# Kernel optimization log

Hardware: AMD Instinct MI355X
Metric: run time of the kernel (lower is better)

## Reference

```python
import jax, jax.numpy as jnp
import numpy as np

B, S, NX = 2, 2048, 1024
N_STATE, N_HEAD = 1024, 16
HEAD_DIM = N_STATE // N_HEAD


def setup_inputs() -> dict:
    key = jax.random.key(0)
    k1, k2, k3 = jax.random.split(key, 3)
    x = jax.random.normal(k1, (B, S, NX), dtype=jnp.float32)
    w_c = jax.random.normal(k2, (NX, 3 * N_STATE), dtype=jnp.float32) * 0.02
    b_c = jnp.zeros((3 * N_STATE,), dtype=jnp.float32)
    w_p = jax.random.normal(k3, (NX, N_STATE), dtype=jnp.float32) * 0.02
    b_p = jnp.zeros((N_STATE,), dtype=jnp.float32)
    return {"x": x, "w_c": w_c, "b_c": b_c, "w_p": w_p, "b_p": b_p}


def reference(x, w_c, b_c, w_p, b_p):
    # c_attn: 1x1 conv == dense over last dim -> [B, S, 3*n_state]
    c = jnp.einsum('bsn,nf->bsf', x, w_c) + b_c
    q, k, v = jnp.split(c, 3, axis=2)

    def split_heads(t):  # [B,S,n_state] -> [B,H,S,D]
        return t.reshape(B, S, N_HEAD, HEAD_DIM).transpose(0, 2, 1, 3)

    q = split_heads(q)
    k = split_heads(k)  # we contract over D directly instead of transposing to [B,H,D,S]
    v = split_heads(v)

    # scores [B,H,S,S], scaled by rsqrt(head_dim) (scale=True)
    w = jnp.einsum('bhqd,bhkd->bhqk', q, k) * jax.lax.rsqrt(jnp.float32(HEAD_DIM))
    # band mask exactly as in source: w*b + -1e9*(1-b)
    band = jnp.tril(jnp.ones((S, S), dtype=jnp.float32))[None, None]
    w = w * band + (-1e9) * (1.0 - band)
    w = jax.nn.softmax(w, axis=-1)
    a = jnp.einsum('bhqk,bhkd->bhqd', w, v)

    # merge heads -> [B,S,n_state]
    a = a.transpose(0, 2, 1, 3).reshape(B, S, N_STATE)
    # c_proj
    out = jnp.einsum('bsn,nf->bsf', a, w_p) + b_p
    return out
```

## Files before the change

kernel.cpp:

```cpp
#include <hip/hip_runtime.h>
#include <math.h>

#define BATCH 2
#define SEQ 2048
#define NX 1024
#define NSTATE 1024
#define NHEAD 16
#define HDIM 64
#define QKV_LD (3*NSTATE)

typedef __attribute__((ext_vector_type(4))) float f32x4;
typedef __attribute__((ext_vector_type(8))) short bf16x8;

__device__ __forceinline__ unsigned short f2bf(float x) {
    unsigned int u = __float_as_uint(x);
    u = (u + 0x7FFFu + ((u >> 16) & 1u)) >> 16;
    return (unsigned short)u;
}

__device__ __forceinline__ unsigned int cvtpk_bf16(float a, float b) {
    unsigned int r;
    asm("v_cvt_pk_bf16_f32 %0, %1, %2" : "=v"(r) : "v"(a), "v"(b));
    return r;
}

#define GLL(src, dst) __builtin_amdgcn_global_load_lds( \
    (const __attribute__((address_space(1))) void*)(src), \
    (__attribute__((address_space(3))) void*)(dst), 16, 0, 0)

__global__ __launch_bounds__(256) void prep_kernel(
    const float* __restrict__ x, const float* __restrict__ w_c,
    const float* __restrict__ w_p,
    unsigned short* __restrict__ xbf, unsigned short* __restrict__ wcT,
    unsigned short* __restrict__ wpT)
{
    const int bx = blockIdx.x;
    const int t = threadIdx.x;
    if (bx < 4096) {
        int i = bx * 256 + t;
        float4 v = ((const float4*)x)[i];
        ushort4 o;
        o.x = f2bf(v.x); o.y = f2bf(v.y); o.z = f2bf(v.z); o.w = f2bf(v.w);
        ((ushort4*)xbf)[i] = o;
        return;
    }
    __shared__ float tile[64][65];
    const float* in;
    unsigned short* out;
    int R, C, c0, r0;
    if (bx < 4096 + 768) {
        int idx = bx - 4096;
        in = w_c; out = wcT; R = NX; C = 3 * NSTATE;
        c0 = (idx % 48) * 64; r0 = (idx / 48) * 64;
    } else {
        int idx = bx - 4864;
        in = w_p; out = wpT; R = NX; C = NSTATE;
        c0 = (idx % 16) * 64; r0 = (idx / 16) * 64;
    }
    const int cc = t & 63;
    const int rb = t >> 6;
    #pragma unroll
    for (int i = 0; i < 16; i++) {
        int rr = rb + i * 4;
        tile[rr][cc] = in[(size_t)(r0 + rr) * C + c0 + cc];
    }
    __syncthreads();
    #pragma unroll
    for (int i = 0; i < 16; i++) {
        int rr = rb + i * 4;
        out[(size_t)(c0 + rr) * R + r0 + cc] = f2bf(tile[cc][rr]);
    }
}

__global__ __launch_bounds__(256) void vtrans_kernel(
    const unsigned short* __restrict__ qkv, unsigned short* __restrict__ vt)
{
    __shared__ unsigned short t[64][72];
    const int s0 = blockIdx.x * 64;
    const int bh = blockIdx.y;
    const int b = bh >> 4, h = bh & 15;
    const int r = threadIdx.x >> 2;
    const int cg = (threadIdx.x & 3) * 16;
    const unsigned short* src = qkv + (size_t)(b * SEQ + s0 + r) * QKV_LD
                                + 2 * NSTATE + h * HDIM + cg;
    *(bf16x8*)&t[r][cg]     = *(const bf16x8*)src;
    *(bf16x8*)&t[r][cg + 8] = *(const bf16x8*)(src + 8);
    __syncthreads();
    unsigned short tmp[16];
    #pragma unroll
    for (int i = 0; i < 16; i++) tmp[i] = t[cg + i][r];
    unsigned short* dst = vt + (size_t)(bh * 64 + r) * SEQ + s0 + cg;
    *(bf16x8*)dst       = ((const bf16x8*)tmp)[0];
    *(bf16x8*)(dst + 8) = ((const bf16x8*)tmp)[1];
}

template<bool BF16_OUT>
__global__ __launch_bounds__(256) void gemm_bf16(
    const unsigned short* __restrict__ A,
    const unsigned short* __restrict__ BT,
    const float* __restrict__ bias,
    void* __restrict__ Cv, int M, int N, int K)
{
    __shared__ unsigned short Als[128 * 32];
    __shared__ unsigned short Bls[128 * 32];
    const int tid = threadIdx.x;
    const int wave = tid >> 6, lane = tid & 63;
    const int bm = blockIdx.x * 128, bn = blockIdx.y * 128;
    const int wr = (wave >> 1) * 64, wc = (wave & 1) * 64;

    f32x4 acc[4][4];
    #pragma unroll
    for (int m = 0; m < 4; m++)
        #pragma unroll
        for (int n = 0; n < 4; n++)
            acc[m][n] = (f32x4){0.f, 0.f, 0.f, 0.f};

    const int arow = tid >> 2;
    const int ac8 = (tid & 3) * 8;
    char* alds0 = (char*)Als + wave * 1024;
    char* blds0 = (char*)Bls + wave * 1024;
    const int fr = lane & 15, kq = (lane >> 4) * 8;

    for (int k0 = 0; k0 < K; k0 += 32) {
        const unsigned short* ga0 = A  + (size_t)(bm + arow) * K + k0 + ac8;
        const unsigned short* gb0 = BT + (size_t)(bn + arow) * K + k0 + ac8;
        GLL(ga0, alds0);
        GLL(ga0 + (size_t)64 * K, alds0 + 4096);
        GLL(gb0, blds0);
        GLL(gb0 + (size_t)64 * K, blds0 + 4096);
        __syncthreads();

        bf16x8 af[4], bfr[4];
        #pragma unroll
        for (int m = 0; m < 4; m++)
            af[m] = *(const bf16x8*)&Als[(wr + m * 16 + fr) * 32 + kq];
        #pragma unroll
        for (int n = 0; n < 4; n++)
            bfr[n] = *(const bf16x8*)&Bls[(wc + n * 16 + fr) * 32 + kq];
        #pragma unroll
        for (int m = 0; m < 4; m++)
            #pragma unroll
            for (int n = 0; n < 4; n++)
                acc[m][n] = __builtin_amdgcn_mfma_f32_16x16x32_bf16(
                    af[m], bfr[n], acc[m][n], 0, 0, 0);
        __syncthreads();
    }

    const int cr = (lane >> 4) * 4;
    const int ccol = lane & 15;
    #pragma unroll
    for (int m = 0; m < 4; m++) {
        const int row = bm + wr + m * 16 + cr;
        #pragma unroll
        for (int n = 0; n < 4; n++) {
            const int col = bn + wc + n * 16 + ccol;
            const float bv = bias[col];
            #pragma unroll
            for (int j = 0; j < 4; j++) {
                float v = acc[m][n][j] + bv;
                if (BF16_OUT)
                    ((unsigned short*)Cv)[(size_t)(row + j) * N + col] = f2bf(v);
                else
                    ((float*)Cv)[(size_t)(row + j) * N + col] = v;
            }
        }
    }
}

__global__ __launch_bounds__(128) void attn_mfma(
    const unsigned short* __restrict__ qkv,
    const unsigned short* __restrict__ vt,
    unsigned short* __restrict__ a_out)
{
    const int cx = blockIdx.x;
    const int h = blockIdx.y, b = blockIdx.z;
    const int tid = threadIdx.x;
    const int w = tid >> 6, lane = tid & 63;
    const int c = lane & 15, hh = lane >> 4;

    __shared__ unsigned short Kls[2 * 64 * 64];
    __shared__ unsigned short Pls[2][16 * 64];

    const float Cc = 0.18033688f;

    const int rr = w * 8 + (lane >> 3);
    const int sc = ((lane & 7) * 16) ^ (((lane >> 3) & 7) << 4);

    const char* gkbase = (const char*)(qkv + (size_t)b * SEQ * QKV_LD + NSTATE + h * HDIM);
    const unsigned short* gv = vt + (size_t)(b * NHEAD + h) * HDIM * SEQ;

    #define STAGE(kt_, buf_) do { \
        const char* gk = gkbase + (size_t)(kt_) * 64 * 6144 + sc; \
        char* kd = (char*)Kls + (buf_) * 8192 + w * 1024; \
        GLL(gk + (size_t)(rr +  0) * 6144, kd); \
        GLL(gk + (size_t)(rr + 16) * 6144, kd + 2048); \
        GLL(gk + (size_t)(rr + 32) * 6144, kd + 4096); \
        GLL(gk + (size_t)(rr + 48) * 6144, kd + 6144); \
    } while (0)

    for (int phase = 0; phase < 2; phase++) {
        const int chunk = phase ? cx : (63 - cx);
        const int rowoff = (chunk & 1) * 32;
        const int qtile = chunk >> 1;

        const size_t qrow = (size_t)(b * SEQ + chunk * 32 + w * 16 + c);
        const unsigned short* qp = qkv + qrow * QKV_LD + h * HDIM;
        bf16x8 qf0 = *(const bf16x8*)(qp + hh * 8);
        bf16x8 qf1 = *(const bf16x8*)(qp + 32 + hh * 8);

        f32x4 acc_o[4];
        #pragma unroll
        for (int n = 0; n < 4; n++) acc_o[n] = (f32x4){0.f, 0.f, 0.f, 0.f};
        float m_run = -1e30f, l = 0.f;

        const int nkt = qtile + 1;
        STAGE(0, 0);
        __syncthreads();

        for (int kt = 0; kt < nkt; kt++) {
            const int cur = kt & 1;
            if (kt + 1 < nkt) STAGE(kt + 1, cur ^ 1);

            bf16x8 vf[4][2];
            #pragma unroll
            for (int n = 0; n < 4; n++)
                #pragma unroll
                for (int hf = 0; hf < 2; hf++)
                    vf[n][hf] = *(const bf16x8*)(gv + (size_t)(n * 16 + c) * SEQ
                                                 + kt * 64 + hf * 32 + hh * 8);

            const char* kb = (const char*)Kls + cur * 8192;

            f32x4 sacc[4];
            __builtin_amdgcn_s_setprio(1);
            #pragma unroll
            for (int m = 0; m < 4; m++) {
                const int row = m * 16 + c;
                const int sw = (row & 7) << 4;
                bf16x8 kf0 = *(const bf16x8*)(kb + row * 128 + ((hh * 16) ^ sw));
                bf16x8 kf1 = *(const bf16x8*)(kb + row * 128 + ((64 + hh * 16) ^ sw));
                f32x4 z = (f32x4){0.f, 0.f, 0.f, 0.f};
                z = __builtin_amdgcn_mfma_f32_16x16x32_bf16(kf0, qf0, z, 0, 0, 0);
                sacc[m] = __builtin_amdgcn_mfma_f32_16x16x32_bf16(kf1, qf1, z, 0, 0, 0);
            }
            __builtin_amdgcn_s_setprio(0);

            const bool diag = (kt == qtile);
            float s[16];
            #pragma unroll
            for (int m = 0; m < 4; m++)
                #pragma unroll
                for (int j = 0; j < 4; j++) {
                    float sv = sacc[m][j];
                    if (diag) {
                        int klocal = m * 16 + hh * 4 + j;
                        if (klocal > rowoff + w * 16 + c) sv = -1e30f;
                    }
                    s[m * 4 + j] = sv;
                }
            float x0 = fmaxf(s[0], s[1]),  x1 = fmaxf(s[2], s[3]);
            float x2 = fmaxf(s[4], s[5]),  x3 = fmaxf(s[6], s[7]);
            float x4 = fmaxf(s[8], s[9]),  x5 = fmaxf(s[10], s[11]);
            float x6 = fmaxf(s[12], s[13]), x7 = fmaxf(s[14], s[15]);
            float y0 = fmaxf(x0, x1), y1 = fmaxf(x2, x3);
            float y2 = fmaxf(x4, x5), y3 = fmaxf(x6, x7);
            float pmax = fmaxf(fmaxf(y0, y1), fmaxf(y2, y3));
            pmax = fmaxf(pmax, __shfl_xor(pmax, 16));
            pmax = fmaxf(pmax, __shfl_xor(pmax, 32));

            if (!__all(pmax <= m_run + 64.0f)) {
                const float mnew = fmaxf(m_run, pmax);
                const float alpha = exp2f((m_run - mnew) * Cc);
                m_run = mnew;
                l *= alpha;
                const float a0 = __shfl(alpha, hh * 4 + 0);
                const float a1 = __shfl(alpha, hh * 4 + 1);
                const float a2 = __shfl(alpha, hh * 4 + 2);
                const float a3 = __shfl(alpha, hh * 4 + 3);
                #pragma unroll
                for (int n = 0; n < 4; n++) {
                    acc_o[n][0] *= a0; acc_o[n][1] *= a1;
                    acc_o[n][2] *= a2; acc_o[n][3] *= a3;
                }
            }
            const float mc = m_run * Cc;
            float p[16];
            #pragma unroll
            for (int i = 0; i < 16; i++)
                p[i] = exp2f(fmaf(s[i], Cc, -mc));
            {
                float a0 = p[0] + p[1],  a1 = p[2] + p[3];
                float a2 = p[4] + p[5],  a3 = p[6] + p[7];
                float a4 = p[8] + p[9],  a5 = p[10] + p[11];
                float a6 = p[12] + p[13], a7 = p[14] + p[15];
                float b0 = a0 + a1, b1 = a2 + a3, b2 = a4 + a5, b3 = a6 + a7;
                l += (b0 + b1) + (b2 + b3);
            }

            {
                char* pb = (char*)&Pls[w][0] + c * 128;
                const int swp = (c & 7) << 4;
                #pragma unroll
                for (int m = 0; m < 4; m++) {
                    uint2 u;
                    u.x = cvtpk_bf16(p[m * 4 + 0], p[m * 4 + 1]);
                    u.y = cvtpk_bf16(p[m * 4 + 2], p[m * 4 + 3]);
                    *(uint2*)(pb + ((m * 32 + hh * 8) ^ swp)) = u;
                }
            }

            {
                const char* pb = (const char*)&Pls[w][0] + c * 128;
                const int swp = (c & 7) << 4;
                bf16x8 pf0 = *(const bf16x8*)(pb + ((hh * 16) ^ swp));
                bf16x8 pf1 = *(const bf16x8*)(pb + ((64 + hh * 16) ^ swp));
                __builtin_amdgcn_s_setprio(1);
                #pragma unroll
                for (int n = 0; n < 4; n++) {
                    acc_o[n] = __builtin_amdgcn_mfma_f32_16x16x32_bf16(pf0, vf[n][0], acc_o[n], 0, 0, 0);
                    acc_o[n] = __builtin_amdgcn_mfma_f32_16x16x32_bf16(pf1, vf[n][1], acc_o[n], 0, 0, 0);
                }
                __builtin_amdgcn_s_setprio(0);
            }
            __syncthreads();
        }

        l += __shfl_xor(l, 16);
        l += __shfl_xor(l, 32);
        const float linv = 1.f / l;
        const float li0 = __shfl(linv, hh * 4 + 0);
        const float li1 = __shfl(linv, hh * 4 + 1);
        const float li2 = __shfl(linv, hh * 4 + 2);
        const float li3 = __shfl(linv, hh * 4 + 3);
        const size_t orow0 = (size_t)(b * SEQ + chunk * 32 + w * 16 + hh * 4);
        #pragma unroll
        for (int n = 0; n < 4; n++) {
            const int col = h * HDIM + n * 16 + c;
            a_out[(orow0 + 0) * NSTATE + col] = f2bf(acc_o[n][0] * li0);
            a_out[(orow0 + 1) * NSTATE + col] = f2bf(acc_o[n][1] * li1);
            a_out[(orow0 + 2) * NSTATE + col] = f2bf(acc_o[n][2] * li2);
            a_out[(orow0 + 3) * NSTATE + col] = f2bf(acc_o[n][3] * li3);
        }
    }
    #undef STAGE
}

extern "C" void kernel_launch(void* const* d_in, const int* in_sizes, int n_in,
                              void* d_out, int out_size, void* d_ws, size_t ws_size,
                              hipStream_t stream)
{
    const float* x   = (const float*)d_in[0];
    const float* w_c = (const float*)d_in[1];
    const float* b_c = (const float*)d_in[2];
    const float* w_p = (const float*)d_in[3];
    const float* b_p = (const float*)d_in[4];
    float* out = (float*)d_out;

    const int M = BATCH * SEQ;

    char* ws = (char*)d_ws;
    unsigned short* qkvbf = (unsigned short*)ws;
    unsigned short* vt    = (unsigned short*)(ws + 25165824);
    unsigned short* xbf   = (unsigned short*)(ws + 25165824 + 8388608);
    unsigned short* wcT   = (unsigned short*)(ws + 25165824 + 2*8388608);
    unsigned short* wpT   = (unsigned short*)(ws + 25165824 + 2*8388608 + 6291456);

    prep_kernel<<<5120, 256, 0, stream>>>(x, w_c, w_p, xbf, wcT, wpT);

    gemm_bf16<true><<<dim3(M / 128, 3 * NSTATE / 128), 256, 0, stream>>>(
        xbf, wcT, b_c, qkvbf, M, 3 * NSTATE, NX);

    vtrans_kernel<<<dim3(SEQ / 64, BATCH * NHEAD), 256, 0, stream>>>(qkvbf, vt);

    attn_mfma<<<dim3(32, NHEAD, BATCH), 128, 0, stream>>>(qkvbf, vt, xbf);

    gemm_bf16<false><<<dim3(M / 128, NSTATE / 128), 256, 0, stream>>>(
        xbf, wpT, b_p, out, M, NSTATE, NX);
}
```

Measured before the change: 233.6 us.

## Split attention into single-wave 16-row blocks with XCD-aware mapping

The attention kernel now runs one 64-thread wave per block over 16 query rows, launched as a flat grid of 4096 blocks. A block index remap groups each (batch, head) onto the same XCD for L2 locality and interleaves short and long causal chunks. K is read straight from global memory into registers instead of being staged through double-buffered LDS, and the block-wide syncs are gone. This gives more parallelism and removes barrier overhead. The cost is that K/V tiles are reused across only 16 query rows, so global and L2 traffic per FLOP roughly doubles.

```diff
diff --git a/kernel.cpp b/kernel.cpp
--- a/kernel.cpp
+++ b/kernel.cpp
@@ -167,182 +167,162 @@
     }
 }
 
-__global__ __launch_bounds__(128) void attn_mfma(
+__global__ __launch_bounds__(64, 4) void attn_mfma(
     const unsigned short* __restrict__ qkv,
     const unsigned short* __restrict__ vt,
     unsigned short* __restrict__ a_out)
 {
-    const int cx = blockIdx.x;
-    const int h = blockIdx.y, b = blockIdx.z;
-    const int tid = threadIdx.x;
-    const int w = tid >> 6, lane = tid & 63;
+    const int beta = blockIdx.x;
+    const int xcd = beta & 7;
+    const int r = beta >> 3;
+    const int g = xcd * 4 + (r & 3);
+    const int s = r >> 2;
+    const int chunk = (s & 1) ? (127 - (s >> 1)) : (s >> 1);
+    const int b = g >> 4, h = g & 15;
+    const int lane = threadIdx.x;
     const int c = lane & 15, hh = lane >> 4;
 
-    __shared__ unsigned short Kls[2 * 64 * 64];
-    __shared__ unsigned short Pls[2][16 * 64];
+    __shared__ unsigned short Pls[16 * 64];
 
     const float Cc = 0.18033688f;
 
-    const int rr = w * 8 + (lane >> 3);
-    const int sc = ((lane & 7) * 16) ^ (((lane >> 3) & 7) << 4);
-
-    const char* gkbase = (const char*)(qkv + (size_t)b * SEQ * QKV_LD + NSTATE + h * HDIM);
-    const unsigned short* gv = vt + (size_t)(b * NHEAD + h) * HDIM * SEQ;
-
-    #define STAGE(kt_, buf_) do { \
-        const char* gk = gkbase + (size_t)(kt_) * 64 * 6144 + sc; \
-        char* kd = (char*)Kls + (buf_) * 8192 + w * 1024; \
-        GLL(gk + (size_t)(rr +  0) * 6144, kd); \
-        GLL(gk + (size_t)(rr + 16) * 6144, kd + 2048); \
-        GLL(gk + (size_t)(rr + 32) * 6144, kd + 4096); \
-        GLL(gk + (size_t)(rr + 48) * 6144, kd + 6144); \
-    } while (0)
-
-    for (int phase = 0; phase < 2; phase++) {
-        const int chunk = phase ? cx : (63 - cx);
-        const int rowoff = (chunk & 1) * 32;
-        const int qtile = chunk >> 1;
-
-        const size_t qrow = (size_t)(b * SEQ + chunk * 32 + w * 16 + c);
-        const unsigned short* qp = qkv + qrow * QKV_LD + h * HDIM;
-        bf16x8 qf0 = *(const bf16x8*)(qp + hh * 8);
-        bf16x8 qf1 = *(const bf16x8*)(qp + 32 + hh * 8);
-
-        f32x4 acc_o[4];
-        #pragma unroll
-        for (int n = 0; n < 4; n++) acc_o[n] = (f32x4){0.f, 0.f, 0.f, 0.f};
-        float m_run = -1e30f, l = 0.f;
-
-        const int nkt = qtile + 1;
-        STAGE(0, 0);
-        __syncthreads();
-
-        for (int kt = 0; kt < nkt; kt++) {
-            const int cur = kt & 1;
-            if (kt + 1 < nkt) STAGE(kt + 1, cur ^ 1);
-
-            bf16x8 vf[4][2];
-            #pragma unroll
-            for (int n = 0; n < 4; n++)
-                #pragma unroll
-                for (int hf = 0; hf < 2; hf++)
-                    vf[n][hf] = *(const bf16x8*)(gv + (size_t)(n * 16 + c) * SEQ
-                                                 + kt * 64 + hf * 32 + hh * 8);
-
-            const char* kb = (const char*)Kls + cur * 8192;
-
-            f32x4 sacc[4];
+    const int qtile = chunk >> 2;
+    const int rowoff = (chunk & 3) * 16;
+    const int nkt = qtile + 1;
+
+    const unsigned short* qp = qkv + (size_t)(b * SEQ + chunk * 16 + c) * QKV_LD + h * HDIM;
+    bf16x8 qf0 = *(const bf16x8*)(qp + hh * 8);
+    bf16x8 qf1 = *(const bf16x8*)(qp + 32 + hh * 8);
+
+    const unsigned short* kbase = qkv + (size_t)b * SEQ * QKV_LD + NSTATE + h * HDIM;
+    const unsigned short* vbase = vt + (size_t)g * HDIM * SEQ;
+
+    f32x4 acc_o[4];
+    #pragma unroll
+    for (int n = 0; n < 4; n++) acc_o[n] = (f32x4){0.f, 0.f, 0.f, 0.f};
+    float m_run = -1e30f, l = 0.f;
+
+    for (int kt = 0; kt < nkt; kt++) {
+        bf16x8 kf[4][2];
+        #pragma unroll
+        for (int m = 0; m < 4; m++) {
+            const unsigned short* kp = kbase + (size_t)(kt * 64 + m * 16 + c) * QKV_LD;
+            kf[m][0] = *(const bf16x8*)(kp + hh * 8);
+            kf[m][1] = *(const bf16x8*)(kp + 32 + hh * 8);
+        }
+        bf16x8 vf[4][2];
+        #pragma unroll
+        for (int n = 0; n < 4; n++) {
+            const unsigned short* vp = vbase + (size_t)(n * 16 + c) * SEQ + kt * 64;
+            vf[n][0] = *(const bf16x8*)(vp + hh * 8);
+            vf[n][1] = *(const bf16x8*)(vp + 32 + hh * 8);
+        }
+
+        f32x4 sacc[4];
+        __builtin_amdgcn_s_setprio(1);
+        #pragma unroll
+        for (int m = 0; m < 4; m++) {
+            f32x4 z = (f32x4){0.f, 0.f, 0.f, 0.f};
+            z = __builtin_amdgcn_mfma_f32_16x16x32_bf16(kf[m][0], qf0, z, 0, 0, 0);
+            sacc[m] = __builtin_amdgcn_mfma_f32_16x16x32_bf16(kf[m][1], qf1, z, 0, 0, 0);
+        }
+        __builtin_amdgcn_s_setprio(0);
+
+        const bool diag = (kt == qtile);
+        float sv_[16];
+        #pragma unroll
+        for (int m = 0; m < 4; m++)
+            #pragma unroll
+            for (int j = 0; j < 4; j++) {
+                float sv = sacc[m][j];
+                if (diag) {
+                    int klocal = m * 16 + hh * 4 + j;
+                    if (klocal > rowoff + c) sv = -1e30f;
+                }
+                sv_[m * 4 + j] = sv;
+            }
+        float x0 = fmaxf(sv_[0], sv_[1]),  x1 = fmaxf(sv_[2], sv_[3]);
+        float x2 = fmaxf(sv_[4], sv_[5]),  x3 = fmaxf(sv_[6], sv_[7]);
+        float x4 = fmaxf(sv_[8], sv_[9]),  x5 = fmaxf(sv_[10], sv_[11]);
+        float x6 = fmaxf(sv_[12], sv_[13]), x7 = fmaxf(sv_[14], sv_[15]);
+        float y0 = fmaxf(x0, x1), y1 = fmaxf(x2, x3);
+        float y2 = fmaxf(x4, x5), y3 = fmaxf(x6, x7);
+        float pmax = fmaxf(fmaxf(y0, y1), fmaxf(y2, y3));
+        pmax = fmaxf(pmax, __shfl_xor(pmax, 16));
+        pmax = fmaxf(pmax, __shfl_xor(pmax, 32));
+
+        if (!__all(pmax <= m_run + 64.0f)) {
+            const float mnew = fmaxf(m_run, pmax);
+            const float alpha = exp2f((m_run - mnew) * Cc);
+            m_run = mnew;
+            l *= alpha;
+            const float a0 = __shfl(alpha, hh * 4 + 0);
+            const float a1 = __shfl(alpha, hh * 4 + 1);
+            const float a2 = __shfl(alpha, hh * 4 + 2);
+            const float a3 = __shfl(alpha, hh * 4 + 3);
+            #pragma unroll
+            for (int n = 0; n < 4; n++) {
+                acc_o[n][0] *= a0; acc_o[n][1] *= a1;
+                acc_o[n][2] *= a2; acc_o[n][3] *= a3;
+            }
+        }
+        const float mc = m_run * Cc;
+        float p[16];
+        #pragma unroll
+        for (int i = 0; i < 16; i++)
+            p[i] = exp2f(fmaf(sv_[i], Cc, -mc));
+        {
+            float a0 = p[0] + p[1],  a1 = p[2] + p[3];
+            float a2 = p[4] + p[5],  a3 = p[6] + p[7];
+            float a4 = p[8] + p[9],  a5 = p[10] + p[11];
+            float a6 = p[12] + p[13], a7 = p[14] + p[15];
+            float b0 = a0 + a1, b1 = a2 + a3, b2 = a4 + a5, b3 = a6 + a7;
+            l += (b0 + b1) + (b2 + b3);
+        }
+
+        {
+            char* pb = (char*)Pls + c * 128;
+            const int swp = (c & 7) << 4;
+            #pragma unroll
+            for (int m = 0; m < 4; m++) {
+                uint2 u;
+                u.x = cvtpk_bf16(p[m * 4 + 0], p[m * 4 + 1]);
+                u.y = cvtpk_bf16(p[m * 4 + 2], p[m * 4 + 3]);
+                *(uint2*)(pb + ((m * 32 + hh * 8) ^ swp)) = u;
+            }
+        }
+
+        {
+            const char* pb = (const char*)Pls + c * 128;
+            const int swp = (c & 7) << 4;
+            bf16x8 pf0 = *(const bf16x8*)(pb + ((hh * 16) ^ swp));
+            bf16x8 pf1 = *(const bf16x8*)(pb + ((64 + hh * 16) ^ swp));
             __builtin_amdgcn_s_setprio(1);
             #pragma unroll
-            for (int m = 0; m < 4; m++) {
-                const int row = m * 16 + c;
-                const int sw = (row & 7) << 4;
-                bf16x8 kf0 = *(const bf16x8*)(kb + row * 128 + ((hh * 16) ^ sw));
-                bf16x8 kf1 = *(const bf16x8*)(kb + row * 128 + ((64 + hh * 16) ^ sw));
-                f32x4 z = (f32x4){0.f, 0.f, 0.f, 0.f};
-                z = __builtin_amdgcn_mfma_f32_16x16x32_bf16(kf0, qf0, z, 0, 0, 0);
-                sacc[m] = __builtin_amdgcn_mfma_f32_16x16x32_bf16(kf1, qf1, z, 0, 0, 0);
+            for (int n = 0; n < 4; n++) {
+                acc_o[n] = __builtin_amdgcn_mfma_f32_16x16x32_bf16(pf0, vf[n][0], acc_o[n], 0, 0, 0);
+                acc_o[n] = __builtin_amdgcn_mfma_f32_16x16x32_bf16(pf1, vf[n][1], acc_o[n], 0, 0, 0);
             }
             __builtin_amdgcn_s_setprio(0);
-
-            const bool diag = (kt == qtile);
-            float s[16];
-            #pragma unroll
-            for (int m = 0; m < 4; m++)
-                #pragma unroll
-                for (int j = 0; j < 4; j++) {
-                    float sv = sacc[m][j];
-                    if (diag) {
-                        int klocal = m * 16 + hh * 4 + j;
-                        if (klocal > rowoff + w * 16 + c) sv = -1e30f;
-                    }
-                    s[m * 4 + j] = sv;
-                }
-            float x0 = fmaxf(s[0], s[1]),  x1 = fmaxf(s[2], s[3]);
-            float x2 = fmaxf(s[4], s[5]),  x3 = fmaxf(s[6], s[7]);
-            float x4 = fmaxf(s[8], s[9]),  x5 = fmaxf(s[10], s[11]);
-            float x6 = fmaxf(s[12], s[13]), x7 = fmaxf(s[14], s[15]);
-            float y0 = fmaxf(x0, x1), y1 = fmaxf(x2, x3);
-            float y2 = fmaxf(x4, x5), y3 = fmaxf(x6, x7);
-            float pmax = fmaxf(fmaxf(y0, y1), fmaxf(y2, y3));
-            pmax = fmaxf(pmax, __shfl_xor(pmax, 16));
-            pmax = fmaxf(pmax, __shfl_xor(pmax, 32));
-
-            if (!__all(pmax <= m_run + 64.0f)) {
-                const float mnew = fmaxf(m_run, pmax);
-                const float alpha = exp2f((m_run - mnew) * Cc);
-                m_run = mnew;
-                l *= alpha;
-                const float a0 = __shfl(alpha, hh * 4 + 0);
-                const float a1 = __shfl(alpha, hh * 4 + 1);
-                const float a2 = __shfl(alpha, hh * 4 + 2);
-                const float a3 = __shfl(alpha, hh * 4 + 3);
-                #pragma unroll
-                for (int n = 0; n < 4; n++) {
-                    acc_o[n][0] *= a0; acc_o[n][1] *= a1;
-                    acc_o[n][2] *= a2; acc_o[n][3] *= a3;
-                }
-            }
-            const float mc = m_run * Cc;
-            float p[16];
-            #pragma unroll
-            for (int i = 0; i < 16; i++)
-                p[i] = exp2f(fmaf(s[i], Cc, -mc));
-            {
-                float a0 = p[0] + p[1],  a1 = p[2] + p[3];
-                float a2 = p[4] + p[5],  a3 = p[6] + p[7];
-                float a4 = p[8] + p[9],  a5 = p[10] + p[11];
-                float a6 = p[12] + p[13], a7 = p[14] + p[15];
-                float b0 = a0 + a1, b1 = a2 + a3, b2 = a4 + a5, b3 = a6 + a7;
-                l += (b0 + b1) + (b2 + b3);
-            }
-
-            {
-                char* pb = (char*)&Pls[w][0] + c * 128;
-                const int swp = (c & 7) << 4;
-                #pragma unroll
-                for (int m = 0; m < 4; m++) {
-                    uint2 u;
-                    u.x = cvtpk_bf16(p[m * 4 + 0], p[m * 4 + 1]);
-                    u.y = cvtpk_bf16(p[m * 4 + 2], p[m * 4 + 3]);
-                    *(uint2*)(pb + ((m * 32 + hh * 8) ^ swp)) = u;
-                }
-            }
-
-            {
-                const char* pb = (const char*)&Pls[w][0] + c * 128;
-                const int swp = (c & 7) << 4;
-                bf16x8 pf0 = *(const bf16x8*)(pb + ((hh * 16) ^ swp));
-                bf16x8 pf1 = *(const bf16x8*)(pb + ((64 + hh * 16) ^ swp));
-                __builtin_amdgcn_s_setprio(1);
-                #pragma unroll
-                for (int n = 0; n < 4; n++) {
-                    acc_o[n] = __builtin_amdgcn_mfma_f32_16x16x32_bf16(pf0, vf[n][0], acc_o[n], 0, 0, 0);
-                    acc_o[n] = __builtin_amdgcn_mfma_f32_16x16x32_bf16(pf1, vf[n][1], acc_o[n], 0, 0, 0);
-                }
-                __builtin_amdgcn_s_setprio(0);
-            }
-            __syncthreads();
-        }
-
-        l += __shfl_xor(l, 16);
-        l += __shfl_xor(l, 32);
-        const float linv = 1.f / l;
-        const float li0 = __shfl(linv, hh * 4 + 0);
-        const float li1 = __shfl(linv, hh * 4 + 1);
-        const float li2 = __shfl(linv, hh * 4 + 2);
-        const float li3 = __shfl(linv, hh * 4 + 3);
-        const size_t orow0 = (size_t)(b * SEQ + chunk * 32 + w * 16 + hh * 4);
-        #pragma unroll
-        for (int n = 0; n < 4; n++) {
-            const int col = h * HDIM + n * 16 + c;
-            a_out[(orow0 + 0) * NSTATE + col] = f2bf(acc_o[n][0] * li0);
-            a_out[(orow0 + 1) * NSTATE + col] = f2bf(acc_o[n][1] * li1);
-            a_out[(orow0 + 2) * NSTATE + col] = f2bf(acc_o[n][2] * li2);
-            a_out[(orow0 + 3) * NSTATE + col] = f2bf(acc_o[n][3] * li3);
-        }
-    }
-    #undef STAGE
+        }
+    }
+
+    l += __shfl_xor(l, 16);
+    l += __shfl_xor(l, 32);
+    const float linv = 1.f / l;
+    const float li0 = __shfl(linv, hh * 4 + 0);
+    const float li1 = __shfl(linv, hh * 4 + 1);
+    const float li2 = __shfl(linv, hh * 4 + 2);
+    const float li3 = __shfl(linv, hh * 4 + 3);
+    const size_t orow0 = (size_t)(b * SEQ + chunk * 16 + hh * 4);
+    #pragma unroll
+    for (int n = 0; n < 4; n++) {
+        const int col = h * HDIM + n * 16 + c;
+        a_out[(orow0 + 0) * NSTATE + col] = f2bf(acc_o[n][0] * li0);
+        a_out[(orow0 + 1) * NSTATE + col] = f2bf(acc_o[n][1] * li1);
+        a_out[(orow0 + 2) * NSTATE + col] = f2bf(acc_o[n][2] * li2);
+        a_out[(orow0 + 3) * NSTATE + col] = f2bf(acc_o[n][3] * li3);
+    }
 }
 
 extern "C" void kernel_launch(void* const* d_in, const int* in_sizes, int n_in,
@@ -372,7 +352,7 @@
 
     vtrans_kernel<<<dim3(SEQ / 64, BATCH * NHEAD), 256, 0, stream>>>(qkvbf, vt);
 
-    attn_mfma<<<dim3(32, NHEAD, BATCH), 128, 0, stream>>>(qkvbf, vt, xbf);
+    attn_mfma<<<4096, 64, 0, stream>>>(qkvbf, vt, xbf);
 
     gemm_bf16<false><<<dim3(M / 128, NSTATE / 128), 256, 0, stream>>>(
         xbf, wpT, b_p, out, M, NSTATE, NX);
```

Result: slower. 326.6 us (+39.8%).
